# Optimization experiments

Hardware: AMD Instinct MI355X
Metric: run time of the kernel (lower is better)

## Reference

```python
import jax, jax.numpy as jnp
import numpy as np

RANK = 3
NUM_STEPS = 3
NUM_ENT = 40000
NUM_EMB = 24
NUM_OPS = 12
DIM = 128
HID = 128
BATCH = 128
NNZ = 300000


def _lstm_dir(x, Wih, Whh, bih, bhh, reverse=False):
    # x: (S, B, D); PyTorch gate order i, f, g, o
    B = x.shape[1]
    H = Whh.shape[1]
    def step(carry, xt):
        h, c = carry
        z = xt @ Wih.T + h @ Whh.T + bih + bhh  # (B, 4H)
        i, f, g, o = jnp.split(z, 4, axis=-1)
        c = jax.nn.sigmoid(f) * c + jax.nn.sigmoid(i) * jnp.tanh(g)
        h = jax.nn.sigmoid(o) * jnp.tanh(c)
        return (h, c), h
    init = (jnp.zeros((B, H), x.dtype), jnp.zeros((B, H), x.dtype))
    _, hs = jax.lax.scan(step, init, x, reverse=reverse)
    return hs  # (S, B, H)


def _spmm(memory, src, dst, val, num_ent):
    # memory: (B, E); edges (src -> dst): out[b, j] = sum_{e: dst[e]=j} memory[b, src[e]] * val[e]
    g = memory[:, src] * val[None, :]              # (B, nnz)
    out = jax.ops.segment_sum(g.T, dst, num_segments=num_ent)  # (E, B)
    return out.T


def setup_inputs() -> dict:
    key = jax.random.key(0)
    ks = jax.random.split(key, 16)
    inp = {
        'queries': jax.random.randint(ks[0], (BATCH,), 0, NUM_EMB),
        'heads': jax.random.randint(ks[1], (BATCH,), 0, NUM_ENT),
        'edge_src': jax.random.randint(ks[2], (NUM_OPS, NNZ), 0, NUM_ENT, dtype=jnp.int32),
        'edge_dst': jax.random.randint(ks[3], (NUM_OPS, NNZ), 0, NUM_ENT, dtype=jnp.int32),
        'edge_val': jax.random.uniform(ks[4], (NUM_OPS, NNZ), jnp.float32),
        'emb': jax.random.normal(ks[5], (NUM_EMB, DIM), jnp.float32) * 0.1,
        'Wih_f': jax.random.normal(ks[6], (RANK, 4 * HID, DIM), jnp.float32) * 0.1,
        'Whh_f': jax.random.normal(ks[7], (RANK, 4 * HID, HID), jnp.float32) * 0.1,
        'bih_f': jnp.zeros((RANK, 4 * HID), jnp.float32),
        'bhh_f': jnp.zeros((RANK, 4 * HID), jnp.float32),
        'Wih_b': jax.random.normal(ks[8], (RANK, 4 * HID, DIM), jnp.float32) * 0.1,
        'Whh_b': jax.random.normal(ks[9], (RANK, 4 * HID, HID), jnp.float32) * 0.1,
        'bih_b': jnp.zeros((RANK, 4 * HID), jnp.float32),
        'bhh_b': jnp.zeros((RANK, 4 * HID), jnp.float32),
        'W0': jax.random.normal(ks[10], (2 * HID, NUM_OPS + 1), jnp.float32) * 0.1,
        'b0': jnp.zeros((1, NUM_OPS + 1), jnp.float32),
    }
    return inp


def reference(queries, heads, edge_src, edge_dst, edge_val, emb,
              Wih_f, Whh_f, bih_f, bhh_f, Wih_b, Whh_b, bih_b, bhh_b, W0, b0):
    # query embedding replicated over time: (S, B, D)
    q = emb[queries]
    x = jnp.broadcast_to(q[None], (NUM_STEPS, q.shape[0], q.shape[1]))
    head_onehot = jax.nn.one_hot(heads, NUM_ENT, dtype=jnp.float32)  # (B, E)

    logits = jnp.zeros((q.shape[0], NUM_ENT), jnp.float32)
    for r in range(RANK):
        hf = _lstm_dir(x, Wih_f[r], Whh_f[r], bih_f[r], bhh_f[r], reverse=False)
        hb = _lstm_dir(x, Wih_b[r], Whh_b[r], bih_b[r], bhh_b[r], reverse=True)
        rnn_out = jnp.concatenate([hf, hb], axis=-1)          # (S, B, 2H)
        trans = rnn_out @ W0 + b0                             # (S, B, ops+1)
        attn = jax.nn.softmax(trans, axis=-1)
        attn = jnp.transpose(attn, (0, 2, 1))                 # (S, ops+1, B)

        memory = head_onehot                                  # (B, E)
        for t in range(NUM_STEPS):
            attn_t = attn[t]                                  # (ops+1, B)
            acc = memory * attn_t[-1][:, None]                # identity operator
            for op in range(NUM_OPS):
                prod = _spmm(memory, edge_src[op], edge_dst[op], edge_val[op], NUM_ENT)
                acc = acc + prod * attn_t[op][:, None]
            memory = acc
        norm = jnp.maximum(jnp.float32(1e-20), jnp.sum(memory, axis=1, keepdims=True))
        logits = logits + memory / norm
    return logits
```

## Files before the change

kernel.cpp:

```cpp
#include <hip/hip_runtime.h>

#define NENT 40000
#define NB 128
#define NQ 24
#define NOPS 12
#define EPO 300000
#define NTOT (NOPS * EPO)
#define NRANK 3
#define NPASS 8
#define CP 16
#define ECAP 160

typedef float v4f __attribute__((ext_vector_type(4)));

__device__ __forceinline__ v4f shfl_xor4(v4f x, int m) {
    v4f r;
    r.x = __shfl_xor(x.x, m);
    r.y = __shfl_xor(x.y, m);
    r.z = __shfl_xor(x.z, m);
    r.w = __shfl_xor(x.w, m);
    return r;
}

__device__ __forceinline__ bool bittest(const unsigned* bm, int i) {
    return (bm[i >> 5] >> (i & 31)) & 1u;
}

__global__ void headmark_kernel(const int* __restrict__ heads, unsigned* __restrict__ bmH,
                                unsigned* __restrict__ bm2) {
    int h = heads[threadIdx.x];
    atomicOr(&bmH[h >> 5], 1u << (h & 31));
    atomicOr(&bm2[h >> 5], 1u << (h & 31));
}

__global__ void mark2_kernel(const int* __restrict__ src, const int* __restrict__ dst,
                             const unsigned* __restrict__ bmH, unsigned* __restrict__ bm2) {
    int i = blockIdx.x * 256 + threadIdx.x;
    if (i < NTOT) {
        int s = src[i];
        if (bittest(bmH, s)) {
            int d = dst[i];
            atomicOr(&bm2[d >> 5], 1u << (d & 31));
        }
    }
}

__global__ void build_ell_kernel(const int* __restrict__ src, const int* __restrict__ dst,
                                 const float* __restrict__ val, const unsigned* __restrict__ bm2,
                                 int* __restrict__ fillD, int* __restrict__ fillS,
                                 int2* __restrict__ eD, int2* __restrict__ eS) {
    int i = blockIdx.x * 256 + threadIdx.x;
    if (i >= NTOT) return;
    int s = src[i], d = dst[i];
    int op = i / EPO;
    int v = __float_as_int(val[i]);
    int pd = atomicAdd(&fillD[d], 1);
    eD[(size_t)d * ECAP + pd] = make_int2(s | (op << 16), v);
    if (bittest(bm2, s)) {
        int ps = atomicAdd(&fillS[s], 1);
        eS[(size_t)s * ECAP + ps] = make_int2(d | (op << 16), v);
    }
}

__global__ void hist_kernel(const int* __restrict__ fillD, int* __restrict__ hist) {
    int j = blockIdx.x * 256 + threadIdx.x;
    if (j < NENT) atomicAdd(&hist[min(fillD[j], 160)], 1);
}

__global__ void prefix_kernel(const int* __restrict__ hist, int* __restrict__ offs) {
    if (threadIdx.x == 0) {
        int s = 0;
        for (int l = 0; l <= 160; ++l) { offs[l] = s; s += hist[l]; }
    }
}

__global__ void scatter_kernel(const int* __restrict__ fillD, int* __restrict__ offs,
                               int* __restrict__ perm) {
    int j = blockIdx.x * 256 + threadIdx.x;
    if (j < NENT) {
        int l = min(fillD[j], 160);
        int p = atomicAdd(&offs[l], 1);
        perm[p] = j;
    }
}

__global__ void lstm_all_kernel(const float* __restrict__ emb,
                                const float* __restrict__ Wih_f, const float* __restrict__ bih_f,
                                const float* __restrict__ bhh_f,
                                const float* __restrict__ Wih_b, const float* __restrict__ bih_b,
                                const float* __restrict__ bhh_b,
                                const float* __restrict__ Whh_f, const float* __restrict__ Whh_b,
                                float* __restrict__ hq) {
    int combo = blockIdx.x / NQ;
    int q = blockIdx.x % NQ;
    int dir = combo / 3, r = combo % 3;
    const float* Wih = (dir ? Wih_b : Wih_f) + r * 512 * 128;
    const float* bih = (dir ? bih_b : bih_f) + r * 512;
    const float* bhh = (dir ? bhh_b : bhh_f) + r * 512;
    const float* Whh = (dir ? Whh_b : Whh_f) + r * 512 * 128;
    __shared__ float x[128];
    __shared__ float h[128];
    int u = threadIdx.x;
    x[u] = emb[q * 128 + u];
    __syncthreads();
    const float* W0p = Wih + u * 128;
    const float* W1p = Wih + (128 + u) * 128;
    const float* W2p = Wih + (256 + u) * 128;
    const float* W3p = Wih + (384 + u) * 128;
    float a0 = 0.f, a1 = 0.f, a2 = 0.f, a3 = 0.f;
    for (int d = 0; d < 128; ++d) {
        float xv = x[d];
        a0 = fmaf(xv, W0p[d], a0);
        a1 = fmaf(xv, W1p[d], a1);
        a2 = fmaf(xv, W2p[d], a2);
        a3 = fmaf(xv, W3p[d], a3);
    }
    float zi0 = a0 + bih[u]       + bhh[u];
    float zf0 = a1 + bih[128 + u] + bhh[128 + u];
    float zg0 = a2 + bih[256 + u] + bhh[256 + u];
    float zo0 = a3 + bih[384 + u] + bhh[384 + u];
    const float* Wi = Whh + u * 128;
    const float* Wf = Whh + (128 + u) * 128;
    const float* Wg = Whh + (256 + u) * 128;
    const float* Wo = Whh + (384 + u) * 128;
    float c = 0.f;
    h[u] = 0.f;
    for (int s = 0; s < 3; ++s) {
        __syncthreads();
        float b0 = 0.f, b1 = 0.f, b2 = 0.f, b3 = 0.f;
        for (int d = 0; d < 128; ++d) {
            float hv = h[d];
            b0 = fmaf(hv, Wi[d], b0);
            b1 = fmaf(hv, Wf[d], b1);
            b2 = fmaf(hv, Wg[d], b2);
            b3 = fmaf(hv, Wo[d], b3);
        }
        float ig = 1.f / (1.f + expf(-(zi0 + b0)));
        float fg = 1.f / (1.f + expf(-(zf0 + b1)));
        float gg = tanhf(zg0 + b2);
        float og = 1.f / (1.f + expf(-(zo0 + b3)));
        c = fg * c + ig * gg;
        float hn = og * tanhf(c);
        __syncthreads();
        h[u] = hn;
        hq[(size_t)((combo * 3 + s) * NQ + q) * 128 + u] = hn;
    }
}

__global__ void attnq_kernel(const float* __restrict__ hq, const float* __restrict__ W0,
                             const float* __restrict__ b0, float* __restrict__ attnq) {
    int r = blockIdx.x / 3, t = blockIdx.x % 3;
    __shared__ float W0s[256 * 13];
    for (int idx = threadIdx.x; idx < 256 * 13; idx += 128) W0s[idx] = W0[idx];
    __syncthreads();
    int q = threadIdx.x;
    if (q >= NQ) return;
    float acc[13];
    for (int k = 0; k < 13; ++k) acc[k] = b0[k];
    const float* hf = hq + (size_t)(((0 * 3 + r) * 3 + t) * NQ + q) * 128;
    const float* hb = hq + (size_t)(((1 * 3 + r) * 3 + (2 - t)) * NQ + q) * 128;
    for (int u = 0; u < 128; ++u) {
        float v = hf[u];
        for (int k = 0; k < 13; ++k) acc[k] = fmaf(v, W0s[u * 13 + k], acc[k]);
    }
    for (int u = 0; u < 128; ++u) {
        float v = hb[u];
        for (int k = 0; k < 13; ++k) acc[k] = fmaf(v, W0s[(128 + u) * 13 + k], acc[k]);
    }
    float m = acc[0];
    for (int k = 1; k < 13; ++k) m = fmaxf(m, acc[k]);
    float e[13];
    float sum = 0.f;
    for (int k = 0; k < 13; ++k) { e[k] = expf(acc[k] - m); sum += e[k]; }
    float inv = 1.f / sum;
    float* ao = attnq + (size_t)(r * 3 + t) * 13 * NQ;
    for (int k = 0; k < 13; ++k) ao[k * NQ + q] = e[k] * inv;
}

__global__ void fused01_kernel(const int* __restrict__ heads, const int* __restrict__ queries,
                               const float* __restrict__ attnq,
                               const int* __restrict__ fillS, const int2* __restrict__ eS,
                               float* __restrict__ mem2) {
    int r = blockIdx.y;
    int b = blockIdx.x;
    int chunk = blockIdx.z;
    __shared__ float c0s[13], c1s[13];
    if (threadIdx.x < 13) {
        int qb = queries[b];
        c0s[threadIdx.x] = attnq[(size_t)((r * 3 + 0) * 13 + threadIdx.x) * NQ + qb];
        c1s[threadIdx.x] = attnq[(size_t)((r * 3 + 1) * 13 + threadIdx.x) * NQ + qb];
    }
    __syncthreads();
    int h = heads[b];
    int lenH = fillS[h];
    float* mem = mem2 + ((size_t)(r * NPASS + (b >> 4)) * NENT) * CP + (b & 15);
    int g = threadIdx.x >> 3, lane8 = threadIdx.x & 7;
    for (int ent = g + chunk * 32; ent < lenH + 1; ent += 64) {
        int i; float wv;
        if (ent == 0) { i = h; wv = c0s[12]; }
        else {
            int2 e = eS[(size_t)h * ECAP + ent - 1];
            i = e.x & 0xFFFF;
            wv = __int_as_float(e.y) * c0s[e.x >> 16];
        }
        if (lane8 == 0) atomicAdd(&mem[(size_t)i * CP], c1s[12] * wv);
        int lenI = fillS[i];
        const int2* ei = eS + (size_t)i * ECAP;
        for (int f = lane8; f < lenI; f += 8) {
            int2 e2 = ei[f];
            atomicAdd(&mem[(size_t)(e2.x & 0xFFFF) * CP],
                      __int_as_float(e2.y) * c1s[e2.x >> 16] * wv);
        }
    }
}

__global__ __launch_bounds__(256) void dense_kernel(const int* __restrict__ queries,
                                                    const float* __restrict__ attnq,
                                                    const int* __restrict__ fillD,
                                                    const int* __restrict__ perm,
                                                    const int2* __restrict__ edgesD,
                                                    const float* __restrict__ in,
                                                    float* __restrict__ out,
                                                    float* __restrict__ normv) {
    int p = blockIdx.x;
    int r = blockIdx.z;
    __shared__ __align__(16) float cs[13 * 20];
    __shared__ float npart[4][16];
    int tid = threadIdx.x;
    if (tid < 13 * 16) {
        int op = tid >> 4, c0 = tid & 15;
        cs[op * 20 + c0] = attnq[(size_t)((r * 3 + 2) * 13 + op) * NQ + queries[p * CP + c0]];
    }
    __syncthreads();
    int wave = tid >> 6, lane = tid & 63;
    int slot = lane >> 2;
    int cq4 = (lane & 3) * 4;
    int jb = blockIdx.y * 16 + wave * 4;
    const float* inr = in + (size_t)(r * NPASS + p) * NENT * CP;
    float* outr = out + (size_t)(r * NPASS + p) * NENT * CP;
    int jr[4], lens[4];
    const int2* edp[4];
#pragma unroll
    for (int t = 0; t < 4; ++t) {
        jr[t] = perm[jb + t];
        lens[t] = fillD[jr[t]];
        edp[t] = edgesD + (size_t)jr[t] * ECAP;
    }
    int maxlen = max(max(lens[0], lens[1]), max(lens[2], lens[3]));
    v4f acc[4];
#pragma unroll
    for (int t = 0; t < 4; ++t) acc[t] = (v4f)0.f;

    for (int base = 0; base < maxlen; base += 32) {
        int2 e[8];
        bool m[8];
#pragma unroll
        for (int t = 0; t < 4; ++t) {
            int ia = base + slot;
            int ib = base + 16 + slot;
            m[t]     = ia < lens[t];
            m[4 + t] = ib < lens[t];
            e[t]     = edp[t][m[t] ? ia : 0];
            e[4 + t] = edp[t][m[4 + t] ? ib : 0];
        }
        v4f g[8];
#pragma unroll
        for (int u = 0; u < 8; ++u) {
            int row = m[u] ? (e[u].x & 0xFFFF) : 0;
            g[u] = *(const v4f*)(inr + (size_t)row * CP + cq4);
        }
#pragma unroll
        for (int u = 0; u < 8; ++u) {
            v4f cc = *(const v4f*)&cs[(e[u].x >> 16) * 20 + cq4];
            float v = m[u] ? __int_as_float(e[u].y) : 0.f;
            acc[u & 3] += (v * cc) * g[u];
        }
    }

    v4f cid = *(const v4f*)&cs[12 * 20 + cq4];
    v4f rsum = (v4f)0.f;
#pragma unroll
    for (int t = 0; t < 4; ++t) {
        v4f red = acc[t];
        red += shfl_xor4(red, 4);
        red += shfl_xor4(red, 8);
        red += shfl_xor4(red, 16);
        red += shfl_xor4(red, 32);
        if (slot == 0) {
            int j = jr[t];
            v4f mi = *(const v4f*)(inr + (size_t)j * CP + cq4);
            v4f res = cid * mi + red;
            *(v4f*)(outr + (size_t)j * CP + cq4) = res;
            rsum += res;
        }
    }
    if (slot == 0) *(v4f*)&npart[wave][cq4] = rsum;
    __syncthreads();
    if (tid < 16) {
        float s = npart[0][tid] + npart[1][tid] + npart[2][tid] + npart[3][tid];
        atomicAdd(&normv[r * 128 + p * CP + tid], s);
    }
}

__global__ void final_kernel(const float* __restrict__ mem3, const float* __restrict__ normv,
                             float* __restrict__ out) {
    __shared__ float tile[32 * 129];
    __shared__ float rn[384];
    for (int idx = threadIdx.x; idx < 384; idx += 256)
        rn[idx] = 1.f / fmaxf(normv[idx], 1e-20f);
    __syncthreads();
    int j0 = blockIdx.x * 32;
    for (int p = 0; p < NPASS; ++p) {
        for (int it = 0; it < 2; ++it) {
            int lin = it * 256 + threadIdx.x;
            int jj = lin >> 4, c = lin & 15;
            int b = p * CP + c;
            float s = 0.f;
            for (int r = 0; r < 3; ++r)
                s += mem3[((size_t)(r * NPASS + p) * NENT + j0 + jj) * CP + c] * rn[r * 128 + b];
            tile[jj * 129 + b] = s;
        }
    }
    __syncthreads();
    for (int it = 0; it < 16; ++it) {
        int lin = it * 256 + threadIdx.x;
        int b = lin >> 5, jj = lin & 31;
        out[(size_t)b * NENT + j0 + jj] = tile[jj * 129 + b];
    }
}

extern "C" void kernel_launch(void* const* d_in, const int* in_sizes, int n_in,
                              void* d_out, int out_size, void* d_ws, size_t ws_size,
                              hipStream_t stream) {
    const int*   queries  = (const int*)d_in[0];
    const int*   heads    = (const int*)d_in[1];
    const int*   edge_src = (const int*)d_in[2];
    const int*   edge_dst = (const int*)d_in[3];
    const float* edge_val = (const float*)d_in[4];
    const float* emb      = (const float*)d_in[5];
    const float* Wih_f    = (const float*)d_in[6];
    const float* Whh_f    = (const float*)d_in[7];
    const float* bih_f    = (const float*)d_in[8];
    const float* bhh_f    = (const float*)d_in[9];
    const float* Wih_b    = (const float*)d_in[10];
    const float* Whh_b    = (const float*)d_in[11];
    const float* bih_b    = (const float*)d_in[12];
    const float* bhh_b    = (const float*)d_in[13];
    const float* W0       = (const float*)d_in[14];
    const float* b0       = (const float*)d_in[15];
    float* out = (float*)d_out;

    char* w = (char*)d_ws;
    size_t off = 0;
    auto alloc = [&](size_t bytes) -> void* {
        off = (off + 255) & ~(size_t)255;
        void* p = w + off;
        off += bytes;
        return p;
    };
    float* attnq  = (float*)alloc((size_t)9 * 13 * NQ * sizeof(float));
    float* hq     = (float*)alloc((size_t)6 * 3 * NQ * 128 * sizeof(float));
    unsigned* bmH = (unsigned*)alloc((2 * 1250 + 2 * NENT + 161) * sizeof(int));
    unsigned* bm2 = bmH + 1250;
    int* fillD    = (int*)(bm2 + 1250);
    int* fillS    = fillD + NENT;
    int* hist     = fillS + NENT;
    int* offs     = (int*)alloc(161 * sizeof(int));
    int* perm     = (int*)alloc((size_t)NENT * sizeof(int));
    int2*  eD     = (int2*)alloc((size_t)NENT * ECAP * sizeof(int2));
    float* mem2   = (float*)alloc((size_t)NRANK * NENT * NB * sizeof(float));
    float* mem3   = (float*)alloc((size_t)NRANK * NENT * NB * sizeof(float));
    int2*  eS     = (int2*)mem3;
    float* normv  = (float*)alloc((size_t)NRANK * NB * sizeof(float));

    int cooGrid = (NTOT + 255) / 256;
    int entGrid = (NENT + 255) / 256;

    hipMemsetAsync(bmH, 0, (2 * 1250 + 2 * NENT + 161) * sizeof(int), stream);
    headmark_kernel<<<1, 128, 0, stream>>>(heads, bmH, bm2);
    mark2_kernel<<<cooGrid, 256, 0, stream>>>(edge_src, edge_dst, bmH, bm2);
    build_ell_kernel<<<cooGrid, 256, 0, stream>>>(edge_src, edge_dst, edge_val, bm2,
                                                  fillD, fillS, eD, eS);

    hist_kernel<<<entGrid, 256, 0, stream>>>(fillD, hist);
    prefix_kernel<<<1, 64, 0, stream>>>(hist, offs);
    scatter_kernel<<<entGrid, 256, 0, stream>>>(fillD, offs, perm);

    lstm_all_kernel<<<6 * NQ, 128, 0, stream>>>(emb, Wih_f, bih_f, bhh_f,
                                                Wih_b, bih_b, bhh_b, Whh_f, Whh_b, hq);
    attnq_kernel<<<9, 128, 0, stream>>>(hq, W0, b0, attnq);

    hipMemsetAsync(mem2, 0, (size_t)NRANK * NENT * NB * sizeof(float), stream);
    hipMemsetAsync(normv, 0, NRANK * NB * sizeof(float), stream);
    {
        dim3 g(NB, NRANK, 2);
        fused01_kernel<<<g, 256, 0, stream>>>(heads, queries, attnq, fillS, eS, mem2);
    }
    {
        dim3 g(NPASS, NENT / 16, NRANK);
        dense_kernel<<<g, 256, 0, stream>>>(queries, attnq, fillD, perm, eD, mem2, mem3, normv);
    }

    final_kernel<<<NENT / 32, 256, 0, stream>>>(mem3, normv, out);
}
```

Baseline: 1.335 ms.

## Compute degree-sorted permutation before ELL build and store rows in sorted order

The per-destination degree count moves into mark2_kernel, and one single-block kernel builds the histogram, a descending-length permutation, slot indices and per-slot lengths. build_ell_kernel then writes each destination's edges straight into its sorted slot, so dense_kernel reads edge rows and lengths contiguously instead of through the perm indirection. This drops two small kernels, the perm-indexed fillD lookup and the scattered row addressing in the dense pass. It adds an extra atomic per edge in mark2 and a serial single-block sort over all entities.

```diff
diff --git a/kernel.cpp b/kernel.cpp
--- a/kernel.cpp
+++ b/kernel.cpp
@@ -34,19 +34,46 @@
 }
 
 __global__ void mark2_kernel(const int* __restrict__ src, const int* __restrict__ dst,
-                             const unsigned* __restrict__ bmH, unsigned* __restrict__ bm2) {
+                             const unsigned* __restrict__ bmH, unsigned* __restrict__ bm2,
+                             int* __restrict__ cntD) {
     int i = blockIdx.x * 256 + threadIdx.x;
     if (i < NTOT) {
+        int d = dst[i];
+        atomicAdd(&cntD[d], 1);
         int s = src[i];
         if (bittest(bmH, s)) {
-            int d = dst[i];
             atomicOr(&bm2[d >> 5], 1u << (d & 31));
         }
+    }
+}
+
+__global__ void sortperm_kernel(const int* __restrict__ cntD, int* __restrict__ perm,
+                                int* __restrict__ slotOf, int* __restrict__ lenS) {
+    __shared__ int hist[161];
+    __shared__ int offs[161];
+    int tid = threadIdx.x;
+    if (tid < 161) hist[tid] = 0;
+    __syncthreads();
+    for (int j = tid; j < NENT; j += 1024)
+        atomicAdd(&hist[min(cntD[j], 160)], 1);
+    __syncthreads();
+    if (tid == 0) {
+        int s = 0;
+        for (int l = 160; l >= 0; --l) { offs[l] = s; s += hist[l]; }
+    }
+    __syncthreads();
+    for (int j = tid; j < NENT; j += 1024) {
+        int l = min(cntD[j], 160);
+        int p = atomicAdd(&offs[l], 1);
+        perm[p] = j;
+        slotOf[j] = p;
+        lenS[p] = l;
     }
 }
 
 __global__ void build_ell_kernel(const int* __restrict__ src, const int* __restrict__ dst,
                                  const float* __restrict__ val, const unsigned* __restrict__ bm2,
+                                 const int* __restrict__ slotOf,
                                  int* __restrict__ fillD, int* __restrict__ fillS,
                                  int2* __restrict__ eD, int2* __restrict__ eS) {
     int i = blockIdx.x * 256 + threadIdx.x;
@@ -55,32 +82,10 @@
     int op = i / EPO;
     int v = __float_as_int(val[i]);
     int pd = atomicAdd(&fillD[d], 1);
-    eD[(size_t)d * ECAP + pd] = make_int2(s | (op << 16), v);
+    eD[(size_t)slotOf[d] * ECAP + pd] = make_int2(s | (op << 16), v);
     if (bittest(bm2, s)) {
         int ps = atomicAdd(&fillS[s], 1);
         eS[(size_t)s * ECAP + ps] = make_int2(d | (op << 16), v);
-    }
-}
-
-__global__ void hist_kernel(const int* __restrict__ fillD, int* __restrict__ hist) {
-    int j = blockIdx.x * 256 + threadIdx.x;
-    if (j < NENT) atomicAdd(&hist[min(fillD[j], 160)], 1);
-}
-
-__global__ void prefix_kernel(const int* __restrict__ hist, int* __restrict__ offs) {
-    if (threadIdx.x == 0) {
-        int s = 0;
-        for (int l = 0; l <= 160; ++l) { offs[l] = s; s += hist[l]; }
-    }
-}
-
-__global__ void scatter_kernel(const int* __restrict__ fillD, int* __restrict__ offs,
-                               int* __restrict__ perm) {
-    int j = blockIdx.x * 256 + threadIdx.x;
-    if (j < NENT) {
-        int l = min(fillD[j], 160);
-        int p = atomicAdd(&offs[l], 1);
-        perm[p] = j;
     }
 }
 
@@ -216,8 +221,8 @@
 
 __global__ __launch_bounds__(256) void dense_kernel(const int* __restrict__ queries,
                                                     const float* __restrict__ attnq,
-                                                    const int* __restrict__ fillD,
                                                     const int* __restrict__ perm,
+                                                    const int* __restrict__ lenS,
                                                     const int2* __restrict__ edgesD,
                                                     const float* __restrict__ in,
                                                     float* __restrict__ out,
@@ -243,8 +248,8 @@
 #pragma unroll
     for (int t = 0; t < 4; ++t) {
         jr[t] = perm[jb + t];
-        lens[t] = fillD[jr[t]];
-        edp[t] = edgesD + (size_t)jr[t] * ECAP;
+        lens[t] = lenS[jb + t];
+        edp[t] = edgesD + (size_t)(jb + t) * ECAP;
     }
     int maxlen = max(max(lens[0], lens[1]), max(lens[2], lens[3]));
     v4f acc[4];
@@ -360,13 +365,14 @@
     };
     float* attnq  = (float*)alloc((size_t)9 * 13 * NQ * sizeof(float));
     float* hq     = (float*)alloc((size_t)6 * 3 * NQ * 128 * sizeof(float));
-    unsigned* bmH = (unsigned*)alloc((2 * 1250 + 2 * NENT + 161) * sizeof(int));
+    unsigned* bmH = (unsigned*)alloc((2 * 1250 + 3 * NENT) * sizeof(int));
     unsigned* bm2 = bmH + 1250;
     int* fillD    = (int*)(bm2 + 1250);
     int* fillS    = fillD + NENT;
-    int* hist     = fillS + NENT;
-    int* offs     = (int*)alloc(161 * sizeof(int));
+    int* cntD     = fillS + NENT;
     int* perm     = (int*)alloc((size_t)NENT * sizeof(int));
+    int* slotOf   = (int*)alloc((size_t)NENT * sizeof(int));
+    int* lenS     = (int*)alloc((size_t)NENT * sizeof(int));
     int2*  eD     = (int2*)alloc((size_t)NENT * ECAP * sizeof(int2));
     float* mem2   = (float*)alloc((size_t)NRANK * NENT * NB * sizeof(float));
     float* mem3   = (float*)alloc((size_t)NRANK * NENT * NB * sizeof(float));
@@ -374,17 +380,13 @@
     float* normv  = (float*)alloc((size_t)NRANK * NB * sizeof(float));
 
     int cooGrid = (NTOT + 255) / 256;
-    int entGrid = (NENT + 255) / 256;
-
-    hipMemsetAsync(bmH, 0, (2 * 1250 + 2 * NENT + 161) * sizeof(int), stream);
+
+    hipMemsetAsync(bmH, 0, (2 * 1250 + 3 * NENT) * sizeof(int), stream);
     headmark_kernel<<<1, 128, 0, stream>>>(heads, bmH, bm2);
-    mark2_kernel<<<cooGrid, 256, 0, stream>>>(edge_src, edge_dst, bmH, bm2);
+    mark2_kernel<<<cooGrid, 256, 0, stream>>>(edge_src, edge_dst, bmH, bm2, cntD);
+    sortperm_kernel<<<1, 1024, 0, stream>>>(cntD, perm, slotOf, lenS);
     build_ell_kernel<<<cooGrid, 256, 0, stream>>>(edge_src, edge_dst, edge_val, bm2,
-                                                  fillD, fillS, eD, eS);
-
-    hist_kernel<<<entGrid, 256, 0, stream>>>(fillD, hist);
-    prefix_kernel<<<1, 64, 0, stream>>>(hist, offs);
-    scatter_kernel<<<entGrid, 256, 0, stream>>>(fillD, offs, perm);
+                                                  slotOf, fillD, fillS, eD, eS);
 
     lstm_all_kernel<<<6 * NQ, 128, 0, stream>>>(emb, Wih_f, bih_f, bhh_f,
                                                 Wih_b, bih_b, bhh_b, Whh_f, Whh_b, hq);
@@ -398,7 +400,7 @@
     }
     {
         dim3 g(NPASS, NENT / 16, NRANK);
-        dense_kernel<<<g, 256, 0, stream>>>(queries, attnq, fillD, perm, eD, mem2, mem3, normv);
+        dense_kernel<<<g, 256, 0, stream>>>(queries, attnq, perm, lenS, eD, mem2, mem3, normv);
     }
 
     final_kernel<<<NENT / 32, 256, 0, stream>>>(mem3, normv, out);
```

Result: slower. 1.453 ms (+8.8%).
